# Kernel tuning notes

Measured on AMD Instinct MI355X. Metric: run time of the kernel, lower is better.

The kernel has to match this reference:

```python
import jax, jax.numpy as jnp
import numpy as np

N_NODES = 100000
N_EDGES = 1000000
F_IN = 64
F_HID = 64
F_OUT = 2
NUM_GRAPHS = 64


def setup_inputs() -> dict:
    key = jax.random.key(0)
    ks = jax.random.split(key, 8)
    x = jax.random.normal(ks[0], (N_NODES, F_IN), dtype=jnp.float32)
    edge_index = jax.random.randint(ks[1], (2, N_EDGES), 0, N_NODES, dtype=jnp.int32)
    batch = jnp.sort(jax.random.randint(ks[2], (N_NODES,), 0, NUM_GRAPHS, dtype=jnp.int32))
    s1 = 1.0 / np.sqrt(F_IN)
    s2 = 1.0 / np.sqrt(F_HID)
    W1 = jax.random.normal(ks[3], (F_IN, F_HID), dtype=jnp.float32) * s1
    W2 = jax.random.normal(ks[4], (F_HID, F_HID), dtype=jnp.float32) * s2
    W3 = jax.random.normal(ks[5], (F_HID, F_HID), dtype=jnp.float32) * s2
    Wlin = jax.random.normal(ks[6], (F_HID, F_OUT), dtype=jnp.float32) * s2
    return {
        "x": x, "edge_index": edge_index, "batch": batch,
        "W1": W1, "b1": jnp.zeros((F_HID,), jnp.float32),
        "W2": W2, "b2": jnp.zeros((F_HID,), jnp.float32),
        "W3": W3, "b3": jnp.zeros((F_HID,), jnp.float32),
        "Wlin": Wlin, "blin": jnp.zeros((F_OUT,), jnp.float32),
    }


def _gcn_norm(edge_index, n_nodes):
    # add self-loops, compute symmetric D^-1/2 (A+I) D^-1/2 edge weights
    loops = jnp.arange(n_nodes, dtype=edge_index.dtype)
    src = jnp.concatenate([edge_index[0], loops])  # message source j
    dst = jnp.concatenate([edge_index[1], loops])  # aggregation target i
    deg = jax.ops.segment_sum(jnp.ones_like(dst, dtype=jnp.float32), dst,
                              num_segments=n_nodes)
    dinv = jnp.where(deg > 0, jax.lax.rsqrt(deg), 0.0)
    norm = dinv[src] * dinv[dst]  # [E+N]
    return src, dst, norm


def _gcn_conv(h, W, b, src, dst, norm, n_nodes):
    h = h @ W                                    # [N, F] dense transform first (PyG order)
    msg = h[src] * norm[:, None]                 # gather + scale  [E+N, F]
    agg = jax.ops.segment_sum(msg, dst, num_segments=n_nodes)
    return agg + b


def reference(x, edge_index, batch, W1, b1, W2, b2, W3, b3, Wlin, blin):
    n = x.shape[0]
    src, dst, norm = _gcn_norm(edge_index, n)
    h = jax.nn.relu(_gcn_conv(x, W1, b1, src, dst, norm, n))
    h = jax.nn.relu(_gcn_conv(h, W2, b2, src, dst, norm, n))
    h = _gcn_conv(h, W3, b3, src, dst, norm, n)
    # global mean pool over graphs
    sums = jax.ops.segment_sum(h, batch, num_segments=NUM_GRAPHS)        # [G, F]
    cnts = jax.ops.segment_sum(jnp.ones((n,), jnp.float32), batch,
                               num_segments=NUM_GRAPHS)
    pooled = sums / jnp.maximum(cnts, 1.0)[:, None]
    # dropout(p=0.1) is identity in eval mode
    return pooled @ Wlin + blin
```

## Files before the change

kernel.cpp:

```cpp
#include <hip/hip_runtime.h>

#define FDIM 64

typedef unsigned short u16;
typedef unsigned int u32;
typedef float v2f __attribute__((ext_vector_type(2)));

__device__ __forceinline__ u16 f2bf(float x) {
    unsigned int u = __float_as_uint(x);
    return (u16)((u + 0x7fff + ((u >> 16) & 1)) >> 16);
}
__device__ __forceinline__ float bf2f(u16 h) {
    return __uint_as_float(((unsigned int)h) << 16);
}
__device__ __forceinline__ u32 pk_fp8x4(float a, float b, float c, float d) {
    u32 p = __builtin_amdgcn_cvt_pk_fp8_f32(a, b, 0, false);
    p = __builtin_amdgcn_cvt_pk_fp8_f32(c, d, p, true);
    return p;
}


template <bool BF16IN, bool SCALE>
__device__ __forceinline__ void mm_tile64(
    const void* __restrict__ ain, const float* __restrict__ bias, int do_relu,
    u32* __restrict__ t, const int* __restrict__ cnt, int n, int blk,
    float (*__restrict__ As)[FDIM + 1], float* __restrict__ Ws)
{
    int tid = threadIdx.x;
    int r0 = blk * 64;

    #pragma unroll
    for (int i = 0; i < 4; ++i) {
        int idx = tid + 256 * i;
        int r = idx >> 4;
        int kq = idx & 15;
        float4 v = make_float4(0.f, 0.f, 0.f, 0.f);
        int R = r0 + r;
        if (R < n) {
            if (BF16IN) {
                ushort4 h = ((const ushort4*)ain)[(size_t)R * 16 + kq];
                v.x = bf2f(h.x); v.y = bf2f(h.y); v.z = bf2f(h.z); v.w = bf2f(h.w);
            } else {
                v = ((const float4*)ain)[(size_t)R * 16 + kq];
            }
            if (bias != nullptr) {
                float4 b = ((const float4*)bias)[kq];
                v.x += b.x; v.y += b.y; v.z += b.z; v.w += b.w;
            }
            if (do_relu) {
                v.x = fmaxf(v.x, 0.f); v.y = fmaxf(v.y, 0.f);
                v.z = fmaxf(v.z, 0.f); v.w = fmaxf(v.w, 0.f);
            }
        }
        As[r][kq * 4 + 0] = v.x;
        As[r][kq * 4 + 1] = v.y;
        As[r][kq * 4 + 2] = v.z;
        As[r][kq * 4 + 3] = v.w;
    }
    __syncthreads();

    int rq = tid >> 4;
    int cq = tid & 15;
    float acc[4][4];
    #pragma unroll
    for (int i = 0; i < 4; ++i)
        #pragma unroll
        for (int j = 0; j < 4; ++j) acc[i][j] = 0.f;

    const float4* Ws4 = (const float4*)Ws;
    #pragma unroll 4
    for (int k = 0; k < FDIM; ++k) {
        float4 w = Ws4[k * 16 + cq];
        float a[4];
        #pragma unroll
        for (int i = 0; i < 4; ++i) a[i] = As[rq * 4 + i][k];
        #pragma unroll
        for (int i = 0; i < 4; ++i) {
            acc[i][0] = fmaf(a[i], w.x, acc[i][0]);
            acc[i][1] = fmaf(a[i], w.y, acc[i][1]);
            acc[i][2] = fmaf(a[i], w.z, acc[i][2]);
            acc[i][3] = fmaf(a[i], w.w, acc[i][3]);
        }
    }

    #pragma unroll
    for (int i = 0; i < 4; ++i) {
        int R = r0 + rq * 4 + i;
        if (R < n) {
            float sc = 1.0f;
            if (SCALE) sc = rsqrtf((float)cnt[R] + 1.0f);
            t[(size_t)R * 16 + cq] =
                pk_fp8x4(acc[i][0] * sc, acc[i][1] * sc,
                         acc[i][2] * sc, acc[i][3] * sc);
        }
    }
}

__global__ __launch_bounds__(256) void k_matmul_h(
    const u16* __restrict__ ain, const float* __restrict__ Wm,
    const float* __restrict__ bias, u32* __restrict__ t,
    const int* __restrict__ cnt, int n)
{
    __shared__ float As[64][FDIM + 1];
    __shared__ float Ws[FDIM * FDIM];
    int tid = threadIdx.x;
    #pragma unroll
    for (int i = 0; i < 4; ++i)
        ((float4*)Ws)[tid + 256 * i] = ((const float4*)Wm)[tid + 256 * i];
    mm_tile64<true, true>(ain, bias, 1, t, cnt, n, blockIdx.x, As, Ws);
}


__global__ __launch_bounds__(256) void k_mm_fill(
    const float* __restrict__ x, const float* __restrict__ W1,
    u32* __restrict__ t,
    const int* __restrict__ src, const int* __restrict__ dst,
    int* __restrict__ cnt, int* __restrict__ csr,
    int n, int E, int cap, int fill_blocks)
{
    __shared__ float As[64][FDIM + 1];
    __shared__ float Ws[FDIM * FDIM];

    int b = blockIdx.x;
    int fb3 = fill_blocks * 3;
    bool fill_role = (b < fb3) && ((b % 3) == 2);

    if (fill_role) {
        int fidx = b / 3;
        int stride = fill_blocks * 256;
        int e = fidx * 256 + threadIdx.x;
        for (; e + 3 * stride < E; e += 4 * stride) {
            int d[4], s[4], p[4];
            #pragma unroll
            for (int u = 0; u < 4; ++u)
                d[u] = __builtin_nontemporal_load(&dst[e + u * stride]);
            #pragma unroll
            for (int u = 0; u < 4; ++u)
                s[u] = __builtin_nontemporal_load(&src[e + u * stride]);
            #pragma unroll
            for (int u = 0; u < 4; ++u) p[u] = atomicAdd(&cnt[d[u]], 1);
            #pragma unroll
            for (int u = 0; u < 4; ++u)
                if (p[u] < cap) csr[(size_t)d[u] * cap + p[u]] = s[u];
        }
        for (; e < E; e += stride) {
            int d = dst[e];
            int p = atomicAdd(&cnt[d], 1);
            if (p < cap) csr[(size_t)d * cap + p] = src[e];
        }
        return;
    }

    int blk = (b < fb3) ? (b - (b + 1) / 3) : (b - fill_blocks);
    int tid = threadIdx.x;
    #pragma unroll
    for (int i = 0; i < 4; ++i)
        ((float4*)Ws)[tid + 256 * i] = ((const float4*)W1)[tid + 256 * i];
    mm_tile64<false, false>(x, nullptr, 0, t, nullptr, n, blk, As, Ws);
}


template <bool SCALED>
__device__ __forceinline__ float4 agg_node(
    int i, const int* __restrict__ cnt, const int* __restrict__ csr,
    const u32* __restrict__ t, int cap, int li, int nbase, int n)
{
    int deg = cnt[i];
    float di = rsqrtf((float)deg + 1.0f);
    int m = deg < cap ? deg : cap;

    u32 sp = t[(size_t)i * 16 + li];
    v2f s0 = __builtin_amdgcn_cvt_pk_f32_fp8(sp, false);
    v2f s1 = __builtin_amdgcn_cvt_pk_f32_fp8(sp, true);
    float4 A0, A1, A2, A3;
    if (SCALED) {
        A0 = make_float4(s0.x, s0.y, s1.x, s1.y);
    } else {
        A0 = make_float4(s0.x * di, s0.y * di, s1.x * di, s1.y * di);
    }
    A1 = make_float4(0.f, 0.f, 0.f, 0.f);
    A2 = make_float4(0.f, 0.f, 0.f, 0.f);
    A3 = make_float4(0.f, 0.f, 0.f, 0.f);

    const int* row = csr + (size_t)i * cap;

    for (int c0 = 0; c0 < m; c0 += 16) {
        int cm = m - c0; if (cm > 16) cm = 16;
        int sv; float dvv = 0.f;
        if (SCALED) {
            sv = (li < cm) ? __builtin_nontemporal_load(&row[c0 + li]) : n;
        } else {
            sv = 0;
            if (li < cm) {
                sv = __builtin_nontemporal_load(&row[c0 + li]);
                dvv = rsqrtf((float)cnt[sv] + 1.0f);
            }
        }
        int jv[16]; float dj[16]; u32 v[16];
        #pragma unroll
        for (int u = 0; u < 16; ++u) {
            jv[u] = __shfl(sv, nbase + u);
            if (!SCALED) dj[u] = __shfl(dvv, nbase + u);
        }
        #pragma unroll
        for (int u = 0; u < 16; ++u) v[u] = t[(size_t)jv[u] * 16 + li];
        #pragma unroll
        for (int u = 0; u < 16; ++u) {
            v2f x0 = __builtin_amdgcn_cvt_pk_f32_fp8(v[u], false);
            v2f x1 = __builtin_amdgcn_cvt_pk_f32_fp8(v[u], true);
            float4* Ap = (u & 3) == 0 ? &A0 : (u & 3) == 1 ? &A1 :
                         (u & 3) == 2 ? &A2 : &A3;
            if (SCALED) {
                Ap->x += x0.x; Ap->y += x0.y;
                Ap->z += x1.x; Ap->w += x1.y;
            } else {
                Ap->x = fmaf(x0.x, dj[u], Ap->x);
                Ap->y = fmaf(x0.y, dj[u], Ap->y);
                Ap->z = fmaf(x1.x, dj[u], Ap->z);
                Ap->w = fmaf(x1.y, dj[u], Ap->w);
            }
        }
    }

    float4 O;
    O.x = ((A0.x + A1.x) + (A2.x + A3.x)) * di;
    O.y = ((A0.y + A1.y) + (A2.y + A3.y)) * di;
    O.z = ((A0.z + A1.z) + (A2.z + A3.z)) * di;
    O.w = ((A0.w + A1.w) + (A2.w + A3.w)) * di;
    return O;
}


template <bool SCALED>
__global__ __launch_bounds__(256) void k_aggregate(
    const int* __restrict__ cnt, const int* __restrict__ csr,
    const u32* __restrict__ t, uint2* __restrict__ aggh, int n, int cap)
{
    int tid = threadIdx.x;
    long long gw = ((long long)blockIdx.x * 256 + tid) >> 6;
    int lane = tid & 63;
    int sub = lane >> 4;
    int li  = lane & 15;
    long long il = gw * 4 + sub;
    if (il >= n) return;
    int i = (int)il;

    float4 O = agg_node<SCALED>(i, cnt, csr, t, cap, li, sub << 4, n);
    uint2 pk;
    pk.x = ((u32)f2bf(O.x)) | (((u32)f2bf(O.y)) << 16);
    pk.y = ((u32)f2bf(O.z)) | (((u32)f2bf(O.w)) << 16);
    aggh[(size_t)i * 16 + li] = pk;
}


__global__ __launch_bounds__(256) void k_agg_pool(
    const int* __restrict__ cnt, const int* __restrict__ csr,
    const u32* __restrict__ t, const int* __restrict__ batch,
    float* __restrict__ partial, int n, int cap, int npart)
{
    int g = blockIdx.x / npart;
    int part = blockIdx.x - g * npart;
    int tid = threadIdx.x;

    int lo = 0, hi = n;
    while (lo < hi) { int mid = (lo + hi) >> 1; if (batch[mid] < g) lo = mid + 1; else hi = mid; }
    int start = lo;
    hi = n;
    while (lo < hi) { int mid = (lo + hi) >> 1; if (batch[mid] <= g) lo = mid + 1; else hi = mid; }
    int end = lo;

    int group = tid >> 4;
    int li = tid & 15;
    int lane = tid & 63;
    int nbase = (lane >> 4) << 4;

    float4 acc = make_float4(0.f, 0.f, 0.f, 0.f);
    for (int i = start + part * 16 + group; i < end; i += npart * 16) {
        float4 O = agg_node<true>(i, cnt, csr, t, cap, li, nbase, n);
        acc.x += O.x; acc.y += O.y; acc.z += O.z; acc.w += O.w;
    }

    __shared__ float4 red[16][16];
    red[group][li] = acc;
    __syncthreads();
    if (tid < 16) {
        float4 s = make_float4(0.f, 0.f, 0.f, 0.f);
        #pragma unroll
        for (int q = 0; q < 16; ++q) {
            s.x += red[q][tid].x; s.y += red[q][tid].y;
            s.z += red[q][tid].z; s.w += red[q][tid].w;
        }
        ((float4*)partial)[((size_t)g * npart + part) * 16 + tid] = s;
    }
}

__global__ __launch_bounds__(64) void k_pool2(
    const float* __restrict__ partial, const int* __restrict__ batch,
    const float* __restrict__ b3, const float* __restrict__ Wlin,
    const float* __restrict__ blin, float* __restrict__ out,
    int n, int fout, int npart)
{
    int g = blockIdx.x;
    int tid = threadIdx.x;

    int lo = 0, hi = n;
    while (lo < hi) { int mid = (lo + hi) >> 1; if (batch[mid] < g) lo = mid + 1; else hi = mid; }
    int start = lo;
    hi = n;
    while (lo < hi) { int mid = (lo + hi) >> 1; if (batch[mid] <= g) lo = mid + 1; else hi = mid; }
    int cnt = lo - start;

    __shared__ float pooled[64];
    float v = 0.f;
    for (int p = 0; p < npart; ++p)
        v += partial[((size_t)g * npart + p) * 64 + tid];
    pooled[tid] = (cnt > 0) ? (v / (float)cnt + b3[tid]) : 0.f;
    __syncthreads();
    if (tid < fout) {
        float o = blin[tid];
        for (int k = 0; k < 64; ++k) o += pooled[k] * Wlin[k * fout + tid];
        out[(size_t)g * fout + tid] = o;
    }
}


extern "C" void kernel_launch(void* const* d_in, const int* in_sizes, int n_in,
                              void* d_out, int out_size, void* d_ws, size_t ws_size,
                              hipStream_t stream) {
    const float* x     = (const float*)d_in[0];
    const int*   ei    = (const int*)d_in[1];
    const int*   batch = (const int*)d_in[2];
    const float* W1 = (const float*)d_in[3];
    const float* b1 = (const float*)d_in[4];
    const float* W2 = (const float*)d_in[5];
    const float* b2 = (const float*)d_in[6];
    const float* W3 = (const float*)d_in[7];
    const float* b3 = (const float*)d_in[8];
    const float* Wl = (const float*)d_in[9];
    const float* bl = (const float*)d_in[10];

    int n = in_sizes[0] / 64;
    int E = in_sizes[1] / 2;
    int fout = in_sizes[10];
    int ngraphs = out_size / fout;

    const int* srcp = ei;
    const int* dstp = ei + E;

    const int npart = 16;

    float* ws   = (float*)d_ws;
    u32*   agg  = (u32*)ws;
    u32*   t    = agg + (size_t)n * 32;
    float* partial = (float*)(t + (size_t)(n + 1) * 16);
    int* cnt    = (int*)(partial + 64 * npart * 64);
    int* csr    = cnt + n;

    size_t fixed = (size_t)n * 32 * 4 + (size_t)(n + 1) * 16 * 4 +
                   64 * npart * 64 * 4 + (size_t)n * 4;
    int cap = 64;
    while (cap > 32 && fixed + (size_t)n * cap * 4 > ws_size) cap -= 8;

    int nb_ag = (int)((((long long)(n + 3) / 4) * 64 + 255) / 256);
    int mm_blocks = (n + 63) / 64;
    int fill_blocks = mm_blocks / 2;
    int total_blocks = mm_blocks + fill_blocks;

    hipMemsetAsync(cnt, 0, (size_t)n * sizeof(int), stream);
    hipMemsetAsync(t + (size_t)n * 16, 0, 64, stream);
    k_mm_fill<<<total_blocks, 256, 0, stream>>>(
        x, W1, t, srcp, dstp, cnt, csr, n, E, cap, fill_blocks);

    k_aggregate<false><<<nb_ag, 256, 0, stream>>>(cnt, csr, t, (uint2*)agg, n, cap);
    k_matmul_h<<<mm_blocks, 256, 0, stream>>>((const u16*)agg, W2, b1, t, cnt, n);
    k_aggregate<true><<<nb_ag, 256, 0, stream>>>(cnt, csr, t, (uint2*)agg, n, cap);
    k_matmul_h<<<mm_blocks, 256, 0, stream>>>((const u16*)agg, W3, b2, t, cnt, n);
    k_agg_pool<<<ngraphs * npart, 256, 0, stream>>>(cnt, csr, t, batch,
                                                    partial, n, cap, npart);
    k_pool2<<<ngraphs, 64, 0, stream>>>(partial, batch, b3, Wl, bl,
                                        (float*)d_out, n, fout, npart);
}
```

Baseline: 270.0 us.

## Pad degree counters per cache line and precompute inverse-sqrt degrees

Each per-node atomic counter gets its own 64-byte slot (stride 16 ints) to reduce atomic contention. A new k_deg kernel compacts the counts and precomputes rsqrt(deg+1) once, and all later kernels read that value instead of recomputing it. The fill/matmul block interleave becomes a fixed 256 fill blocks placed first, with the edge loop unrolled by 8. The cost is a 16x larger counter memset, an extra kernel launch, and more workspace, which may reduce the available CSR cap.

```diff
diff --git a/kernel.cpp b/kernel.cpp
--- a/kernel.cpp
+++ b/kernel.cpp
@@ -1,6 +1,7 @@
 #include <hip/hip_runtime.h>
 
 #define FDIM 64
+#define CPAD 16
 
 typedef unsigned short u16;
 typedef unsigned int u32;
@@ -23,7 +24,7 @@
 template <bool BF16IN, bool SCALE>
 __device__ __forceinline__ void mm_tile64(
     const void* __restrict__ ain, const float* __restrict__ bias, int do_relu,
-    u32* __restrict__ t, const int* __restrict__ cnt, int n, int blk,
+    u32* __restrict__ t, const float* __restrict__ dinv, int n, int blk,
     float (*__restrict__ As)[FDIM + 1], float* __restrict__ Ws)
 {
     int tid = threadIdx.x;
@@ -88,7 +89,7 @@
         int R = r0 + rq * 4 + i;
         if (R < n) {
             float sc = 1.0f;
-            if (SCALE) sc = rsqrtf((float)cnt[R] + 1.0f);
+            if (SCALE) sc = dinv[R];
             t[(size_t)R * 16 + cq] =
                 pk_fp8x4(acc[i][0] * sc, acc[i][1] * sc,
                          acc[i][2] * sc, acc[i][3] * sc);
@@ -99,7 +100,7 @@
 __global__ __launch_bounds__(256) void k_matmul_h(
     const u16* __restrict__ ain, const float* __restrict__ Wm,
     const float* __restrict__ bias, u32* __restrict__ t,
-    const int* __restrict__ cnt, int n)
+    const float* __restrict__ dinv, int n)
 {
     __shared__ float As[64][FDIM + 1];
     __shared__ float Ws[FDIM * FDIM];
@@ -107,7 +108,7 @@
     #pragma unroll
     for (int i = 0; i < 4; ++i)
         ((float4*)Ws)[tid + 256 * i] = ((const float4*)Wm)[tid + 256 * i];
-    mm_tile64<true, true>(ain, bias, 1, t, cnt, n, blockIdx.x, As, Ws);
+    mm_tile64<true, true>(ain, bias, 1, t, dinv, n, blockIdx.x, As, Ws);
 }
 
 
@@ -115,43 +116,38 @@
     const float* __restrict__ x, const float* __restrict__ W1,
     u32* __restrict__ t,
     const int* __restrict__ src, const int* __restrict__ dst,
-    int* __restrict__ cnt, int* __restrict__ csr,
+    int* __restrict__ pcnt, int* __restrict__ csr,
     int n, int E, int cap, int fill_blocks)
 {
     __shared__ float As[64][FDIM + 1];
     __shared__ float Ws[FDIM * FDIM];
 
-    int b = blockIdx.x;
-    int fb3 = fill_blocks * 3;
-    bool fill_role = (b < fb3) && ((b % 3) == 2);
-
-    if (fill_role) {
-        int fidx = b / 3;
+    if ((int)blockIdx.x < fill_blocks) {
         int stride = fill_blocks * 256;
-        int e = fidx * 256 + threadIdx.x;
-        for (; e + 3 * stride < E; e += 4 * stride) {
-            int d[4], s[4], p[4];
+        int e = blockIdx.x * 256 + threadIdx.x;
+        for (; e + 7 * stride < E; e += 8 * stride) {
+            int d[8], s[8], p[8];
             #pragma unroll
-            for (int u = 0; u < 4; ++u)
+            for (int u = 0; u < 8; ++u)
                 d[u] = __builtin_nontemporal_load(&dst[e + u * stride]);
             #pragma unroll
-            for (int u = 0; u < 4; ++u)
+            for (int u = 0; u < 8; ++u)
                 s[u] = __builtin_nontemporal_load(&src[e + u * stride]);
             #pragma unroll
-            for (int u = 0; u < 4; ++u) p[u] = atomicAdd(&cnt[d[u]], 1);
+            for (int u = 0; u < 8; ++u) p[u] = atomicAdd(&pcnt[(size_t)d[u] * CPAD], 1);
             #pragma unroll
-            for (int u = 0; u < 4; ++u)
+            for (int u = 0; u < 8; ++u)
                 if (p[u] < cap) csr[(size_t)d[u] * cap + p[u]] = s[u];
         }
         for (; e < E; e += stride) {
             int d = dst[e];
-            int p = atomicAdd(&cnt[d], 1);
+            int p = atomicAdd(&pcnt[(size_t)d * CPAD], 1);
             if (p < cap) csr[(size_t)d * cap + p] = src[e];
         }
         return;
     }
 
-    int blk = (b < fb3) ? (b - (b + 1) / 3) : (b - fill_blocks);
+    int blk = blockIdx.x - fill_blocks;
     int tid = threadIdx.x;
     #pragma unroll
     for (int i = 0; i < 4; ++i)
@@ -159,15 +155,28 @@
     mm_tile64<false, false>(x, nullptr, 0, t, nullptr, n, blk, As, Ws);
 }
 
+__global__ __launch_bounds__(256) void k_deg(
+    const int* __restrict__ pcnt, int* __restrict__ deg,
+    float* __restrict__ dinv, int n)
+{
+    int i = blockIdx.x * 256 + threadIdx.x;
+    if (i < n) {
+        int c = pcnt[(size_t)i * CPAD];
+        deg[i] = c;
+        dinv[i] = rsqrtf((float)c + 1.0f);
+    }
+}
+
 
 template <bool SCALED>
 __device__ __forceinline__ float4 agg_node(
-    int i, const int* __restrict__ cnt, const int* __restrict__ csr,
-    const u32* __restrict__ t, int cap, int li, int nbase, int n)
-{
-    int deg = cnt[i];
-    float di = rsqrtf((float)deg + 1.0f);
-    int m = deg < cap ? deg : cap;
+    int i, const int* __restrict__ deg, const float* __restrict__ dinv,
+    const int* __restrict__ csr, const u32* __restrict__ t,
+    int cap, int li, int nbase, int n)
+{
+    int dg = deg[i];
+    float di = dinv[i];
+    int m = dg < cap ? dg : cap;
 
     u32 sp = t[(size_t)i * 16 + li];
     v2f s0 = __builtin_amdgcn_cvt_pk_f32_fp8(sp, false);
@@ -193,7 +202,7 @@
             sv = 0;
             if (li < cm) {
                 sv = __builtin_nontemporal_load(&row[c0 + li]);
-                dvv = rsqrtf((float)cnt[sv] + 1.0f);
+                dvv = dinv[sv];
             }
         }
         int jv[16]; float dj[16]; u32 v[16];
@@ -233,8 +242,9 @@
 
 template <bool SCALED>
 __global__ __launch_bounds__(256) void k_aggregate(
-    const int* __restrict__ cnt, const int* __restrict__ csr,
-    const u32* __restrict__ t, uint2* __restrict__ aggh, int n, int cap)
+    const int* __restrict__ deg, const float* __restrict__ dinv,
+    const int* __restrict__ csr, const u32* __restrict__ t,
+    uint2* __restrict__ aggh, int n, int cap)
 {
     int tid = threadIdx.x;
     long long gw = ((long long)blockIdx.x * 256 + tid) >> 6;
@@ -245,7 +255,7 @@
     if (il >= n) return;
     int i = (int)il;
 
-    float4 O = agg_node<SCALED>(i, cnt, csr, t, cap, li, sub << 4, n);
+    float4 O = agg_node<SCALED>(i, deg, dinv, csr, t, cap, li, sub << 4, n);
     uint2 pk;
     pk.x = ((u32)f2bf(O.x)) | (((u32)f2bf(O.y)) << 16);
     pk.y = ((u32)f2bf(O.z)) | (((u32)f2bf(O.w)) << 16);
@@ -254,9 +264,10 @@
 
 
 __global__ __launch_bounds__(256) void k_agg_pool(
-    const int* __restrict__ cnt, const int* __restrict__ csr,
-    const u32* __restrict__ t, const int* __restrict__ batch,
-    float* __restrict__ partial, int n, int cap, int npart)
+    const int* __restrict__ deg, const float* __restrict__ dinv,
+    const int* __restrict__ csr, const u32* __restrict__ t,
+    const int* __restrict__ batch, float* __restrict__ partial,
+    int n, int cap, int npart)
 {
     int g = blockIdx.x / npart;
     int part = blockIdx.x - g * npart;
@@ -276,7 +287,7 @@
 
     float4 acc = make_float4(0.f, 0.f, 0.f, 0.f);
     for (int i = start + part * 16 + group; i < end; i += npart * 16) {
-        float4 O = agg_node<true>(i, cnt, csr, t, cap, li, nbase, n);
+        float4 O = agg_node<true>(i, deg, dinv, csr, t, cap, li, nbase, n);
         acc.x += O.x; acc.y += O.y; acc.z += O.z; acc.w += O.w;
     }
 
@@ -353,29 +364,33 @@
     u32*   agg  = (u32*)ws;
     u32*   t    = agg + (size_t)n * 32;
     float* partial = (float*)(t + (size_t)(n + 1) * 16);
-    int* cnt    = (int*)(partial + 64 * npart * 64);
-    int* csr    = cnt + n;
+    int* pcnt   = (int*)(partial + 64 * npart * 64);
+    int* deg    = pcnt + (size_t)n * CPAD;
+    float* dinv = (float*)(deg + n);
+    int* csr    = (int*)(dinv + n);
 
     size_t fixed = (size_t)n * 32 * 4 + (size_t)(n + 1) * 16 * 4 +
-                   64 * npart * 64 * 4 + (size_t)n * 4;
+                   64 * npart * 64 * 4 + (size_t)n * CPAD * 4 +
+                   (size_t)n * 4 + (size_t)n * 4;
     int cap = 64;
     while (cap > 32 && fixed + (size_t)n * cap * 4 > ws_size) cap -= 8;
 
     int nb_ag = (int)((((long long)(n + 3) / 4) * 64 + 255) / 256);
     int mm_blocks = (n + 63) / 64;
-    int fill_blocks = mm_blocks / 2;
-    int total_blocks = mm_blocks + fill_blocks;
-
-    hipMemsetAsync(cnt, 0, (size_t)n * sizeof(int), stream);
+    int fill_blocks = 256;
+
+    hipMemsetAsync(pcnt, 0, (size_t)n * CPAD * sizeof(int), stream);
     hipMemsetAsync(t + (size_t)n * 16, 0, 64, stream);
-    k_mm_fill<<<total_blocks, 256, 0, stream>>>(
-        x, W1, t, srcp, dstp, cnt, csr, n, E, cap, fill_blocks);
-
-    k_aggregate<false><<<nb_ag, 256, 0, stream>>>(cnt, csr, t, (uint2*)agg, n, cap);
-    k_matmul_h<<<mm_blocks, 256, 0, stream>>>((const u16*)agg, W2, b1, t, cnt, n);
-    k_aggregate<true><<<nb_ag, 256, 0, stream>>>(cnt, csr, t, (uint2*)agg, n, cap);
-    k_matmul_h<<<mm_blocks, 256, 0, stream>>>((const u16*)agg, W3, b2, t, cnt, n);
-    k_agg_pool<<<ngraphs * npart, 256, 0, stream>>>(cnt, csr, t, batch,
+    k_mm_fill<<<fill_blocks + mm_blocks, 256, 0, stream>>>(
+        x, W1, t, srcp, dstp, pcnt, csr, n, E, cap, fill_blocks);
+
+    k_deg<<<(n + 255) / 256, 256, 0, stream>>>(pcnt, deg, dinv, n);
+
+    k_aggregate<false><<<nb_ag, 256, 0, stream>>>(deg, dinv, csr, t, (uint2*)agg, n, cap);
+    k_matmul_h<<<mm_blocks, 256, 0, stream>>>((const u16*)agg, W2, b1, t, dinv, n);
+    k_aggregate<true><<<nb_ag, 256, 0, stream>>>(deg, dinv, csr, t, (uint2*)agg, n, cap);
+    k_matmul_h<<<mm_blocks, 256, 0, stream>>>((const u16*)agg, W3, b2, t, dinv, n);
+    k_agg_pool<<<ngraphs * npart, 256, 0, stream>>>(deg, dinv, csr, t, batch,
                                                     partial, n, cap, npart);
     k_pool2<<<ngraphs, 64, 0, stream>>>(partial, batch, b3, Wl, bl,
                                         (float*)d_out, n, fout, npart);
```

Result: no change. 268.8 us (-0.4%).
